# Performance work log

Hardware: AMD Instinct MI355X
Metric: run time of the kernel (lower is better)

## Reference

```python
import jax, jax.numpy as jnp
import numpy as np

STRIDE = 32
ANCHOR_SCALES = (16, 32, 64)
RATIOS = (0.5, 1.0, 2.0)
BASE_SIZE = 16
A = 9                    # base_anchors
PRE_NMS_TOP_N = 6000
POST_NMS_TOP_N = 1000
NMS_THRESH = 0.7
MIN_SIZE = 16.0


def _base_anchors():
    w = h = float(BASE_SIZE)
    cx = cy = (BASE_SIZE - 1) * 0.5
    out = []
    for r in RATIOS:
        ws = np.round(np.sqrt(w * h / r))
        hs = np.round(ws * r)
        for s in ANCHOR_SCALES:
            W_, H_ = ws * s, hs * s
            out.append([cx - 0.5 * (W_ - 1), cy - 0.5 * (H_ - 1),
                        cx + 0.5 * (W_ - 1), cy + 0.5 * (H_ - 1)])
    return np.asarray(out, dtype=np.float32)  # [9,4]


def _conv(x, w, b, padding):
    y = jax.lax.conv_general_dilated(x, w, (1, 1), padding,
                                     dimension_numbers=('NCHW', 'OIHW', 'NCHW'))
    return y + b[None, :, None, None]


def reference(features, rpn_w, rpn_b, cls_w, cls_b, box_w, box_b, image_height, image_width):
    H, W = features.shape[2], features.shape[3]
    x = jax.nn.relu(_conv(features, rpn_w, rpn_b, 'SAME'))
    cls_score = _conv(x, cls_w, cls_b, 'VALID')           # [1,2A,H,W]
    cls_prob = jax.nn.softmax(cls_score, axis=1)           # nn.Softmax2d: softmax over all 2A channels
    bbox_pred = _conv(x, box_w, box_b, 'VALID')            # [1,4A,H,W]

    scores = cls_prob[0, A:].transpose(1, 2, 0).reshape(-1)       # fg scores [H*W*A]
    deltas = bbox_pred[0].transpose(1, 2, 0).reshape(-1, 4)        # [H*W*A,4]

    base = jnp.asarray(_base_anchors())
    sx = jnp.arange(W, dtype=jnp.float32) * STRIDE
    sy = jnp.arange(H, dtype=jnp.float32) * STRIDE
    sxx, syy = jnp.meshgrid(sx, sy)                                # [H,W]
    shifts = jnp.stack([sxx, syy, sxx, syy], axis=-1).reshape(-1, 4)
    anchors = (shifts[:, None, :] + base[None, :, :]).reshape(-1, 4)

    # bbox_transform_inv decode
    wa = anchors[:, 2] - anchors[:, 0] + 1.0
    ha = anchors[:, 3] - anchors[:, 1] + 1.0
    cxa = anchors[:, 0] + 0.5 * (wa - 1.0)
    cya = anchors[:, 1] + 0.5 * (ha - 1.0)
    cx = deltas[:, 0] * wa + cxa
    cy = deltas[:, 1] * ha + cya
    pw = wa * jnp.exp(deltas[:, 2])
    ph = ha * jnp.exp(deltas[:, 3])
    x1 = jnp.clip(cx - 0.5 * pw, 0.0, image_width - 1.0)
    y1 = jnp.clip(cy - 0.5 * ph, 0.0, image_height - 1.0)
    x2 = jnp.clip(cx + 0.5 * pw, 0.0, image_width - 1.0)
    y2 = jnp.clip(cy + 0.5 * ph, 0.0, image_height - 1.0)
    boxes = jnp.stack([x1, y1, x2, y2], axis=-1)

    valid0 = ((x2 - x1 + 1.0) >= MIN_SIZE) & ((y2 - y1 + 1.0) >= MIN_SIZE)
    scores = jnp.where(valid0, scores, -jnp.inf)

    top_scores, top_idx = jax.lax.top_k(scores, PRE_NMS_TOP_N)
    tb = boxes[top_idx]                                             # [P,4]
    tx1, ty1, tx2, ty2 = tb[:, 0], tb[:, 1], tb[:, 2], tb[:, 3]
    areas = (tx2 - tx1 + 1.0) * (ty2 - ty1 + 1.0)
    xx1 = jnp.maximum(tx1[:, None], tx1[None, :])
    yy1 = jnp.maximum(ty1[:, None], ty1[None, :])
    xx2 = jnp.minimum(tx2[:, None], tx2[None, :])
    yy2 = jnp.minimum(ty2[:, None], ty2[None, :])
    inter = jnp.maximum(xx2 - xx1 + 1.0, 0.0) * jnp.maximum(yy2 - yy1 + 1.0, 0.0)
    iou = inter / (areas[:, None] + areas[None, :] - inter)         # [P,P]

    def step(state, _):
        alive, = (state,) if not isinstance(state, tuple) else (None,)
        return state, None

    def nms_step(state, _):
        alive, sel_list = state
        s = jnp.where(alive, top_scores, -jnp.inf)
        j = jnp.argmax(s)
        ok = s[j] > -jnp.inf
        alive = alive & (jnp.take(iou, j, axis=0) <= NMS_THRESH)    # suppresses j too (iou=1)
        return (alive, sel_list), (j.astype(jnp.int32), ok)

    alive0 = jnp.isfinite(top_scores)
    (_, _), (sel, selv) = jax.lax.scan(nms_step, (alive0, 0),
                                       jnp.arange(POST_NMS_TOP_N), length=POST_NMS_TOP_N)

    out_boxes = tb[sel] * selv[:, None].astype(tb.dtype)            # zero-pad invalid slots
    rois = jnp.concatenate([jnp.zeros((POST_NMS_TOP_N, 1), tb.dtype), out_boxes], axis=1)
    return rois                                                     # [POST_NMS_TOP_N, 5]


def setup_inputs() -> dict:
    key = jax.random.key(0)
    ks = jax.random.split(key, 4)
    features = jax.random.normal(ks[0], (1, 256, 128, 128), dtype=jnp.float32)
    rpn_w = 0.01 * jax.random.normal(ks[1], (256, 256, 3, 3), dtype=jnp.float32)
    rpn_b = jnp.zeros((256,), jnp.float32)
    cls_w = 0.01 * jax.random.normal(ks[2], (18, 256, 1, 1), dtype=jnp.float32)
    cls_b = jnp.zeros((18,), jnp.float32)
    box_w = 0.01 * jax.random.normal(ks[3], (36, 256, 1, 1), dtype=jnp.float32)
    box_b = jnp.zeros((36,), jnp.float32)
    return {'features': features, 'rpn_w': rpn_w, 'rpn_b': rpn_b,
            'cls_w': cls_w, 'cls_b': cls_b, 'box_w': box_w, 'box_b': box_b,
            'image_height': 4096, 'image_width': 4096}
```

## Files before the change

### kernel.cpp

```cpp
#include <hip/hip_runtime.h>
#include <stdint.h>
#include <math.h>

typedef unsigned long long u64;
typedef unsigned int u32;
typedef float float4a __attribute__((ext_vector_type(4), aligned(4)));
typedef unsigned long long u64x2 __attribute__((ext_vector_type(2), aligned(16)));

static const size_t OFF_CTL   = 0;
static const size_t OFF_HIST  = 1024;
static const size_t OFF_DOTS  = 1049600;
static const size_t OFF_WCV   = 4588544;
static const size_t OFF_XD    = 6947840;
static const size_t OFF_BOX   = 23725056;
static const size_t OFF_KEYS  = 26084352;
static const size_t OFF_CKEY  = 27264000;
static const size_t OFF_CIDX  = 27313152;
static const size_t OFF_TB    = 27337728;
static const size_t OFF_TSC   = 27433728;
static const size_t OFF_ALIVE = 27458048;
static const size_t OFF_FPAD  = 32067584;
static const size_t OFF_MASKP = OFF_FPAD;

__device__ __forceinline__ float exp_xla(float x) {
    float m = floorf(__fmaf_rn(x, 1.44269504088896341f, 0.5f));
    float r = __fmaf_rn(m, -0.693359375f, x);
    r = __fmaf_rn(m, 2.12194440e-4f, r);
    float r2 = r * r;
    float p = 1.9875691500e-4f;
    p = __fmaf_rn(p, r, 1.3981999507e-3f);
    p = __fmaf_rn(p, r, 8.3334519073e-3f);
    p = __fmaf_rn(p, r, 4.1665795894e-2f);
    p = __fmaf_rn(p, r, 1.6666665459e-1f);
    p = __fmaf_rn(p, r, 5.0000001201e-1f);
    p = __fmaf_rn(p, r2, r);
    p = __fadd_rn(p, 1.0f);
    int mi = (int)m;
    return p * __int_as_float((mi + 127) << 23);
}

__device__ __forceinline__ void gload_lds16(const void* g, void* l) {
    __builtin_amdgcn_global_load_lds(
        (const __attribute__((address_space(1))) void*)g,
        (__attribute__((address_space(3))) void*)l, 16, 0, 0);
}

__global__ void prep_wcv(const float* __restrict__ rpn_w, float* __restrict__ wcv) {
    int t = blockIdx.x * 256 + threadIdx.x;
    if (t >= 589824) return;
    int tap = t / 65536, rem = t % 65536, ic = rem / 256, oc = rem % 256;
    wcv[t] = rpn_w[oc * 2304 + ic * 9 + tap];
}

__global__ void prep_pad(const float* __restrict__ feat, float* __restrict__ featP) {
    int t = blockIdx.x * 256 + threadIdx.x;
    if (t >= 256 * 130 * 132) return;
    int ic = t / 17160, rem = t % 17160, y = rem / 132, x = rem % 132;
    int sy = y - 1, sx = x - 1;
    float v = 0.f;
    if (sy >= 0 && sy < 128 && sx >= 0 && sx < 128)
        v = feat[ic * 16384 + sy * 128 + sx];
    featP[t] = v;
}

__global__ __launch_bounds__(256, 2) void conv3x3(const float* __restrict__ featP,
                                                  const float* __restrict__ wcv,
                                                  const float* __restrict__ rpn_b,
                                                  float* __restrict__ xd) {
    __shared__ float sW[8192];
    const int band = blockIdx.x & 7;
    const int slot = blockIdx.x >> 3;
    const int tx = slot & 7, ocb = slot >> 3;
    const int oc0 = ocb * 32;
    const int tid = threadIdx.x;
    const int wid = tid >> 6;
    const int lane = tid & 63;
    const int py = lane >> 2, px0 = (lane & 3) * 4;
    const int gy = band * 16 + py, gx0 = tx * 16 + px0;
    const int ocB = oc0 + wid * 8;
    float acc[4][8];
#pragma unroll
    for (int p = 0; p < 4; ++p)
#pragma unroll
        for (int o = 0; o < 8; ++o) acc[p][o] = 0.f;
#pragma unroll
    for (int tap = 0; tap < 9; ++tap) {
        __syncthreads();
        for (int idx = tid; idx < 8192; idx += 256)
            sW[idx] = wcv[tap * 65536 + (idx >> 5) * 256 + oc0 + (idx & 31)];
        __syncthreads();
        const float* fp = featP + (size_t)(gy + tap / 3) * 132 + (gx0 + tap % 3);
        const float* wl = sW + wid * 8;
#pragma unroll 4
        for (int ic = 0; ic < 256; ++ic) {
            float4a fA = *(const float4a*)(fp + (size_t)ic * 17160);
            float4a w0 = *(const float4a*)(wl + ic * 32);
            float4a w1 = *(const float4a*)(wl + ic * 32 + 4);
#pragma unroll
            for (int p = 0; p < 4; ++p) {
#pragma unroll
                for (int o = 0; o < 4; ++o)
                    acc[p][o] = __fmaf_rn(fA[p], w0[o], acc[p][o]);
#pragma unroll
                for (int o = 0; o < 4; ++o)
                    acc[p][4 + o] = __fmaf_rn(fA[p], w1[o], acc[p][4 + o]);
            }
        }
    }
#pragma unroll
    for (int p = 0; p < 4; ++p) {
        float* op = xd + (size_t)(gy * 128 + gx0 + p) * 256 + ocB;
#pragma unroll
        for (int o = 0; o < 8; ++o) {
            float v = __fadd_rn(acc[p][o], rpn_b[ocB + o]);
            op[o] = v > 0.f ? v : 0.f;
        }
    }
}

__global__ __launch_bounds__(256, 1) void heads_seq(const float* __restrict__ xd,
                                                    const float* __restrict__ cls_w,
                                                    const float* __restrict__ box_w,
                                                    float* __restrict__ dots) {
    __shared__ float sX[4][260];
    const int tid = threadIdx.x;
    const int pix0 = blockIdx.x * 4;
    for (int idx = tid; idx < 1024; idx += 256)
        sX[idx >> 8][idx & 255] = xd[(size_t)(pix0 + (idx >> 8)) * 256 + (idx & 255)];
    __syncthreads();
    if (tid < 216) {
        const int pl = tid / 54, o = tid % 54;
        const float* wr = (o < 18) ? (cls_w + o * 256) : (box_w + (o - 18) * 256);
        const float4* x4 = (const float4*)&sX[pl][0];
        const float4* w4 = (const float4*)wr;
        float acc = 0.f;
        for (int q = 0; q < 64; ++q) {
            float4 xv = x4[q];
            float4 wv = w4[q];
            acc = __fmaf_rn(xv.x, wv.x, acc);
            acc = __fmaf_rn(xv.y, wv.y, acc);
            acc = __fmaf_rn(xv.z, wv.z, acc);
            acc = __fmaf_rn(xv.w, wv.w, acc);
        }
        dots[(size_t)(pix0 + pl) * 54 + o] = acc;
    }
}

__global__ __launch_bounds__(256, 1) void decode(const float* __restrict__ dots,
                                                 const float* __restrict__ cls_b,
                                                 const float* __restrict__ box_b,
                                                 float4* __restrict__ boxes,
                                                 u64* __restrict__ keys) {
    const int pix = blockIdx.x * 256 + threadIdx.x;
    if (pix >= 16384) return;
    const float* dt = dots + (size_t)pix * 54;
    float d[54];
#pragma unroll
    for (int i = 0; i < 54; ++i)
        d[i] = __fadd_rn(dt[i], (i < 18 ? cls_b[i] : box_b[i - 18]));
    float m = d[0];
#pragma unroll
    for (int i = 1; i < 18; ++i) m = fmaxf(m, d[i]);
    float e[18];
#pragma unroll
    for (int i = 0; i < 18; ++i) e[i] = exp_xla(__fsub_rn(d[i], m));
    float s = e[0];
#pragma unroll
    for (int i = 1; i < 18; ++i) s = __fadd_rn(s, e[i]);
    const int y = pix >> 7, x = pix & 127;
    const float shx = (float)(x * 32), shy = (float)(y * 32);
    const float AW[9] = {368.f, 736.f, 1472.f, 256.f, 512.f, 1024.f, 176.f, 352.f, 704.f};
    const float AH[9] = {192.f, 384.f, 768.f, 256.f, 512.f, 1024.f, 352.f, 704.f, 1408.f};
#pragma unroll
    for (int a = 0; a < 9; ++a) {
        float score = e[9 + a] / s;
        float wa = AW[a], ha = AH[a];
        float cxa = __fadd_rn(shx, 7.5f), cya = __fadd_rn(shy, 7.5f);
        float dx = d[18 + 4 * a], dyy = d[19 + 4 * a];
        float dw = d[20 + 4 * a], dh = d[21 + 4 * a];
        float cx = __fadd_rn(__fmul_rn(dx, wa), cxa);
        float cy = __fadd_rn(__fmul_rn(dyy, ha), cya);
        float pw = __fmul_rn(wa, exp_xla(dw));
        float ph = __fmul_rn(ha, exp_xla(dh));
        float hx = __fmul_rn(0.5f, pw), hy = __fmul_rn(0.5f, ph);
        float x1 = fminf(fmaxf(__fsub_rn(cx, hx), 0.f), 4095.f);
        float y1 = fminf(fmaxf(__fsub_rn(cy, hy), 0.f), 4095.f);
        float x2 = fminf(fmaxf(__fadd_rn(cx, hx), 0.f), 4095.f);
        float y2 = fminf(fmaxf(__fadd_rn(cy, hy), 0.f), 4095.f);
        float vw = __fadd_rn(__fsub_rn(x2, x1), 1.0f);
        float vh = __fadd_rn(__fsub_rn(y2, y1), 1.0f);
        bool valid = (vw >= 16.0f) && (vh >= 16.0f);
        int i = pix * 9 + a;
        boxes[i] = make_float4(x1, y1, x2, y2);
        u64 k;
        if (valid) {
            u32 b = __float_as_uint(score);
            k = ((u64)(u32)~(b | 0x80000000u) << 32) | (u32)i;
        } else {
            k = (0xFFFFFFFFULL << 32) | (u32)i;
        }
        keys[i] = k;
    }
}

__global__ __launch_bounds__(256) void hist_scan(const u64* __restrict__ keys,
                                                 u32* __restrict__ ghist,
                                                 u64* pfx, u32* tgt,
                                                 u32* done, int pass) {
    __shared__ u32 lh[256];
    __shared__ u32 lastFlag;
    __shared__ u32 h[256];
    __shared__ u32 incl[256];
    const int t = threadIdx.x;
    lh[t] = 0;
    if (t == 0) lastFlag = 0;
    __syncthreads();
    const u64 pref = *pfx;
    const u32 target0 = (pass == 0) ? 6000u : *tgt;
    const int shift = 56 - 8 * pass;
    for (int i = blockIdx.x * 256 + t; i < 147456; i += 64 * 256) {
        u64 k = keys[i];
        bool match = (pass == 0) || ((k >> (shift + 8)) == pref);
        if (match) atomicAdd(&lh[(u32)(k >> shift) & 0xFFu], 1u);
    }
    __syncthreads();
    if (lh[t]) atomicAdd(&ghist[t], lh[t]);
    __threadfence();
    __syncthreads();
    if (t == 0) {
        u32 prev = atomicAdd(done, 1u);
        if (prev == 63) lastFlag = 1;
    }
    __syncthreads();
    if (!lastFlag) return;
    u32 hv = atomicAdd(&ghist[t], 0u);
    h[t] = hv;
    incl[t] = hv;
    __syncthreads();
    for (int off = 1; off < 256; off <<= 1) {
        u32 v = (t >= off) ? incl[t - off] : 0u;
        __syncthreads();
        incl[t] += v;
        __syncthreads();
    }
    u64 p0 = (pass == 0) ? 0ULL : pref;
    u32 before = incl[t] - h[t];
    if (before < target0 && target0 <= incl[t]) {
        *pfx = (p0 << 8) | (u64)t;
        *tgt = target0 - before;
    }
}

__global__ void compact(const u64* __restrict__ keys, const u64* __restrict__ kstar,
                        u32* count, u64* __restrict__ ckey, u32* __restrict__ cidx) {
    int i = blockIdx.x * 256 + threadIdx.x;
    if (i >= 147456) return;
    u64 k = keys[i];
    if (k <= *kstar) {
        u32 pos = atomicAdd(count, 1u);
        if (pos < 6144) { ckey[pos] = k; cidx[pos] = (u32)(k & 0xFFFFFFFFu); }
    }
}

__global__ __launch_bounds__(256) void rank_scatter(const u64* __restrict__ ckey,
                                                    const u32* __restrict__ cidx,
                                                    const u32* __restrict__ count,
                                                    const float4* __restrict__ boxes,
                                                    float4* __restrict__ tb,
                                                    float* __restrict__ tsc) {
    __shared__ u64 LK[6144];
    int N = (int)*count; if (N > 6144) N = 6144;
    for (int i = threadIdx.x; i < N; i += 256) LK[i] = ckey[i];
    __syncthreads();
    int e = blockIdx.x * 256 + threadIdx.x;
    if (e >= N) return;
    u64 myK = LK[e];
    u32 myI = cidx[e];
    int rank = 0;
    for (int c = 0; c < N; ++c) rank += (LK[c] < myK);
    if (rank < 6000) {
        tb[rank] = boxes[myI];
        u32 hi = (u32)(myK >> 32);
        tsc[rank] = (hi == 0xFFFFFFFFu) ? -__builtin_inff()
                                        : __uint_as_float(~hi & 0x7FFFFFFFu);
    }
}

__global__ void alive_init(const float* __restrict__ tsc, u64* __restrict__ alive0) {
    int r = blockIdx.x * 256 + threadIdx.x;
    bool a = false;
    if (r < 6000) a = tsc[r] > -__builtin_inff();
    u64 b = __ballot(a);
    if ((threadIdx.x & 63) == 0) alive0[r >> 6] = b;
}

__global__ __launch_bounds__(256) void nms_mask(const float4* __restrict__ tb,
                                                u64* __restrict__ mask) {
    int tid = blockIdx.x * 256 + threadIdx.x;
    if (tid >= 6000 * 94) return;
    int j = tid / 94, w = tid % 94;
    float4 bj = tb[j];
    float arJ = __fmul_rn(__fadd_rn(__fsub_rn(bj.z, bj.x), 1.0f),
                          __fadd_rn(__fsub_rn(bj.w, bj.y), 1.0f));
    u64 m = 0;
    int base = w * 64;
#pragma unroll 4
    for (int b = 0; b < 64; ++b) {
        int i = base + b;
        if (i >= 6000) break;
        float4 bi = tb[i];
        float arI = __fmul_rn(__fadd_rn(__fsub_rn(bi.z, bi.x), 1.0f),
                              __fadd_rn(__fsub_rn(bi.w, bi.y), 1.0f));
        float xx1 = fmaxf(bj.x, bi.x), yy1 = fmaxf(bj.y, bi.y);
        float xx2 = fminf(bj.z, bi.z), yy2 = fminf(bj.w, bi.w);
        float ww = fmaxf(__fadd_rn(__fsub_rn(xx2, xx1), 1.0f), 0.0f);
        float hh = fmaxf(__fadd_rn(__fsub_rn(yy2, yy1), 1.0f), 0.0f);
        float inter = __fmul_rn(ww, hh);
        float uni = __fsub_rn(__fadd_rn(arJ, arI), inter);
        float iou = inter / uni;
        if (iou > 0.7f) m |= (1ULL << b);
    }
    mask[(size_t)j * 128 + 2 * (w & 63) + (w >> 6)] = m;
}

__global__ __launch_bounds__(64, 1) void nms_seq(const u64* __restrict__ alive0,
                                                 const u64* __restrict__ mask,
                                                 const float4* __restrict__ tb,
                                                 float* __restrict__ out) {
    __shared__ __align__(16) u64 lwin[2][64 * 128];
    __shared__ u32 sel[1000];
    const int lane = threadIdx.x;
    u64 wl = alive0[lane];
    u64 wh = (lane < 30) ? alive0[64 + lane] : 0ULL;
    int base = -1000000;
    int pbase = -1;
    int cur = 0;
    int k = 0;
    for (; k < 1000; ++k) {
        int j;
        {
            u64 blo = __ballot(wl != 0ULL);
            if (blo) {
                int l = __ffsll((long long)blo) - 1;
                u32 a = __builtin_amdgcn_readlane((u32)wl, l);
                u32 b = __builtin_amdgcn_readlane((u32)(wl >> 32), l);
                u64 w = ((u64)b << 32) | (u64)a;
                j = l * 64 + __ffsll((long long)w) - 1;
            } else {
                u64 bhi = __ballot(wh != 0ULL);
                if (!bhi) break;
                int l = __ffsll((long long)bhi) - 1;
                u32 a = __builtin_amdgcn_readlane((u32)wh, l);
                u32 b = __builtin_amdgcn_readlane((u32)(wh >> 32), l);
                u64 w = ((u64)b << 32) | (u64)a;
                j = (64 + l) * 64 + __ffsll((long long)w) - 1;
            }
        }
        if (lane == 0) sel[k] = (u32)j;
        if (j >= base + 64) {
            if (pbase >= 0 && j < pbase + 64) {
                asm volatile("s_waitcnt vmcnt(0)" ::: "memory");
                cur ^= 1;
                base = pbase;
            } else {
                int js = (j > 5936) ? 5936 : j;
                asm volatile("s_waitcnt vmcnt(0)" ::: "memory");
                const char* gsrc = (const char*)mask + (size_t)js * 1024 + (size_t)lane * 16;
                char* ldst = (char*)&lwin[cur][0];
#pragma unroll
                for (int i = 0; i < 64; ++i)
                    gload_lds16(gsrc + (size_t)i * 1024, ldst + i * 1024);
                base = js;
                asm volatile("s_waitcnt vmcnt(0)" ::: "memory");
            }
            pbase = -1;
            if (base + 64 < 6000) {
                int ps = (base + 64 > 5936) ? 5936 : (base + 64);
                const char* gs2 = (const char*)mask + (size_t)ps * 1024 + (size_t)lane * 16;
                char* ld2 = (char*)&lwin[cur ^ 1][0];
#pragma unroll
                for (int i = 0; i < 64; ++i)
                    gload_lds16(gs2 + (size_t)i * 1024, ld2 + i * 1024);
                pbase = ps;
            }
        }
        const int s = j - base;
        u64x2 rd = *(const u64x2*)&lwin[cur][(size_t)s * 128 + 2 * lane];
        u64 rl = rd.x;
        u64 rh = rd.y;
        wl &= ~rl;
        if (lane < 30) wh &= ~rh;
    }
    __syncthreads();
    for (int r = lane; r < k; r += 64) {
        int j = (int)sel[r];
        float4 bj = tb[j];
        out[r * 5 + 1] = bj.x;
        out[r * 5 + 2] = bj.y;
        out[r * 5 + 3] = bj.z;
        out[r * 5 + 4] = bj.w;
    }
}

extern "C" void kernel_launch(void* const* d_in, const int* in_sizes, int n_in,
                              void* d_out, int out_size, void* d_ws, size_t ws_size,
                              hipStream_t stream) {
    const float *feat = nullptr, *rpn_w = nullptr, *rpn_b = nullptr;
    const float *cls_w = nullptr, *cls_b = nullptr, *box_w = nullptr, *box_b = nullptr;
    for (int i = 0; i < n_in; ++i) {
        switch (in_sizes[i]) {
            case 4194304: feat  = (const float*)d_in[i]; break;
            case 589824:  rpn_w = (const float*)d_in[i]; break;
            case 256:     rpn_b = (const float*)d_in[i]; break;
            case 4608:    cls_w = (const float*)d_in[i]; break;
            case 18:      cls_b = (const float*)d_in[i]; break;
            case 9216:    box_w = (const float*)d_in[i]; break;
            case 36:      box_b = (const float*)d_in[i]; break;
            default: break;
        }
    }

    char* w = (char*)d_ws;
    u64* pfx       = (u64*)(w + OFF_CTL);
    u32* tgt       = (u32*)(w + OFF_CTL + 8);
    u32* ctlCount  = (u32*)(w + OFF_CTL + 12);
    u32* done      = (u32*)(w + OFF_CTL + 16);
    u32* hist      = (u32*)(w + OFF_HIST);
    float* dots    = (float*)(w + OFF_DOTS);
    float* wcv     = (float*)(w + OFF_WCV);
    float* xd      = (float*)(w + OFF_XD);
    float4* boxes  = (float4*)(w + OFF_BOX);
    u64* keys      = (u64*)(w + OFF_KEYS);
    u64* ckey      = (u64*)(w + OFF_CKEY);
    u32* cidx      = (u32*)(w + OFF_CIDX);
    float4* tb     = (float4*)(w + OFF_TB);
    float* tsc     = (float*)(w + OFF_TSC);
    u64* alive0    = (u64*)(w + OFF_ALIVE);
    u64* maskP     = (u64*)(w + OFF_MASKP);
    float* featP   = (float*)(w + OFF_FPAD);

    hipMemsetAsync(d_ws, 0, OFF_HIST + 8 * 256 * 4, stream);
    hipMemsetAsync(d_out, 0, (size_t)out_size * sizeof(float), stream);

    prep_wcv<<<2304, 256, 0, stream>>>(rpn_w, wcv);
    prep_pad<<<17160, 256, 0, stream>>>(feat, featP);
    conv3x3<<<512, 256, 0, stream>>>(featP, wcv, rpn_b, xd);
    heads_seq<<<4096, 256, 0, stream>>>(xd, cls_w, box_w, dots);
    decode<<<64, 256, 0, stream>>>(dots, cls_b, box_b, boxes, keys);
    for (int p = 0; p < 8; ++p)
        hist_scan<<<64, 256, 0, stream>>>(keys, hist + p * 256, pfx, tgt, done + p, p);
    compact<<<576, 256, 0, stream>>>(keys, pfx, ctlCount, ckey, cidx);
    rank_scatter<<<24, 256, 0, stream>>>(ckey, cidx, ctlCount, boxes, tb, tsc);
    alive_init<<<24, 256, 0, stream>>>(tsc, alive0);
    nms_mask<<<2204, 256, 0, stream>>>(tb, maskP);
    nms_seq<<<1, 64, 0, stream>>>(alive0, maskP, tb, (float*)d_out);
}
```

Measured before the change: 904.6 us.

## Fuse head dots with decode, halve radix-select passes, fold alive init into scatter

```diff
diff --git a/kernel.cpp b/kernel.cpp
--- a/kernel.cpp
+++ b/kernel.cpp
@@ -17,7 +17,6 @@
 static const size_t OFF_CKEY  = 27264000;
 static const size_t OFF_CIDX  = 27313152;
 static const size_t OFF_TB    = 27337728;
-static const size_t OFF_TSC   = 27433728;
 static const size_t OFF_ALIVE = 27458048;
 static const size_t OFF_FPAD  = 32067584;
 static const size_t OFF_MASKP = OFF_FPAD;
@@ -118,11 +117,15 @@
     }
 }
 
-__global__ __launch_bounds__(256, 1) void heads_seq(const float* __restrict__ xd,
-                                                    const float* __restrict__ cls_w,
-                                                    const float* __restrict__ box_w,
-                                                    float* __restrict__ dots) {
+__global__ __launch_bounds__(256, 1) void heads_decode(const float* __restrict__ xd,
+                                                       const float* __restrict__ cls_w,
+                                                       const float* __restrict__ box_w,
+                                                       const float* __restrict__ cls_b,
+                                                       const float* __restrict__ box_b,
+                                                       float4* __restrict__ boxes,
+                                                       u64* __restrict__ keys) {
     __shared__ float sX[4][260];
+    __shared__ float sD[4][54];
     const int tid = threadIdx.x;
     const int pix0 = blockIdx.x * 4;
     for (int idx = tid; idx < 1024; idx += 256)
@@ -142,18 +145,13 @@
             acc = __fmaf_rn(xv.z, wv.z, acc);
             acc = __fmaf_rn(xv.w, wv.w, acc);
         }
-        dots[(size_t)(pix0 + pl) * 54 + o] = acc;
-    }
-}
-
-__global__ __launch_bounds__(256, 1) void decode(const float* __restrict__ dots,
-                                                 const float* __restrict__ cls_b,
-                                                 const float* __restrict__ box_b,
-                                                 float4* __restrict__ boxes,
-                                                 u64* __restrict__ keys) {
-    const int pix = blockIdx.x * 256 + threadIdx.x;
-    if (pix >= 16384) return;
-    const float* dt = dots + (size_t)pix * 54;
+        sD[pl][o] = acc;
+    }
+    __syncthreads();
+    if (tid >= 36) return;
+    const int pl = tid / 9, a = tid % 9;
+    const int pix = pix0 + pl;
+    const float* dt = sD[pl];
     float d[54];
 #pragma unroll
     for (int i = 0; i < 54; ++i)
@@ -171,36 +169,33 @@
     const float shx = (float)(x * 32), shy = (float)(y * 32);
     const float AW[9] = {368.f, 736.f, 1472.f, 256.f, 512.f, 1024.f, 176.f, 352.f, 704.f};
     const float AH[9] = {192.f, 384.f, 768.f, 256.f, 512.f, 1024.f, 352.f, 704.f, 1408.f};
-#pragma unroll
-    for (int a = 0; a < 9; ++a) {
-        float score = e[9 + a] / s;
-        float wa = AW[a], ha = AH[a];
-        float cxa = __fadd_rn(shx, 7.5f), cya = __fadd_rn(shy, 7.5f);
-        float dx = d[18 + 4 * a], dyy = d[19 + 4 * a];
-        float dw = d[20 + 4 * a], dh = d[21 + 4 * a];
-        float cx = __fadd_rn(__fmul_rn(dx, wa), cxa);
-        float cy = __fadd_rn(__fmul_rn(dyy, ha), cya);
-        float pw = __fmul_rn(wa, exp_xla(dw));
-        float ph = __fmul_rn(ha, exp_xla(dh));
-        float hx = __fmul_rn(0.5f, pw), hy = __fmul_rn(0.5f, ph);
-        float x1 = fminf(fmaxf(__fsub_rn(cx, hx), 0.f), 4095.f);
-        float y1 = fminf(fmaxf(__fsub_rn(cy, hy), 0.f), 4095.f);
-        float x2 = fminf(fmaxf(__fadd_rn(cx, hx), 0.f), 4095.f);
-        float y2 = fminf(fmaxf(__fadd_rn(cy, hy), 0.f), 4095.f);
-        float vw = __fadd_rn(__fsub_rn(x2, x1), 1.0f);
-        float vh = __fadd_rn(__fsub_rn(y2, y1), 1.0f);
-        bool valid = (vw >= 16.0f) && (vh >= 16.0f);
-        int i = pix * 9 + a;
-        boxes[i] = make_float4(x1, y1, x2, y2);
-        u64 k;
-        if (valid) {
-            u32 b = __float_as_uint(score);
-            k = ((u64)(u32)~(b | 0x80000000u) << 32) | (u32)i;
-        } else {
-            k = (0xFFFFFFFFULL << 32) | (u32)i;
-        }
-        keys[i] = k;
-    }
+    float score = e[9 + a] / s;
+    float wa = AW[a], ha = AH[a];
+    float cxa = __fadd_rn(shx, 7.5f), cya = __fadd_rn(shy, 7.5f);
+    float dx = d[18 + 4 * a], dyy = d[19 + 4 * a];
+    float dw = d[20 + 4 * a], dh = d[21 + 4 * a];
+    float cx = __fadd_rn(__fmul_rn(dx, wa), cxa);
+    float cy = __fadd_rn(__fmul_rn(dyy, ha), cya);
+    float pw = __fmul_rn(wa, exp_xla(dw));
+    float ph = __fmul_rn(ha, exp_xla(dh));
+    float hx = __fmul_rn(0.5f, pw), hy = __fmul_rn(0.5f, ph);
+    float x1 = fminf(fmaxf(__fsub_rn(cx, hx), 0.f), 4095.f);
+    float y1 = fminf(fmaxf(__fsub_rn(cy, hy), 0.f), 4095.f);
+    float x2 = fminf(fmaxf(__fadd_rn(cx, hx), 0.f), 4095.f);
+    float y2 = fminf(fmaxf(__fadd_rn(cy, hy), 0.f), 4095.f);
+    float vw = __fadd_rn(__fsub_rn(x2, x1), 1.0f);
+    float vh = __fadd_rn(__fsub_rn(y2, y1), 1.0f);
+    bool valid = (vw >= 16.0f) && (vh >= 16.0f);
+    int i = pix * 9 + a;
+    boxes[i] = make_float4(x1, y1, x2, y2);
+    u64 k;
+    if (valid) {
+        u32 b = __float_as_uint(score);
+        k = ((u64)(u32)~(b | 0x80000000u) << 32) | (u32)i;
+    } else {
+        k = (0xFFFFFFFFULL << 32) | (u32)i;
+    }
+    keys[i] = k;
 }
 
 __global__ __launch_bounds__(256) void hist_scan(const u64* __restrict__ keys,
@@ -252,11 +247,13 @@
 }
 
 __global__ void compact(const u64* __restrict__ keys, const u64* __restrict__ kstar,
-                        u32* count, u64* __restrict__ ckey, u32* __restrict__ cidx) {
+                        u32* count, u64* __restrict__ ckey, u32* __restrict__ cidx,
+                        u64* __restrict__ alive0) {
+    if (blockIdx.x == 0 && threadIdx.x < 128) alive0[threadIdx.x] = 0ULL;
     int i = blockIdx.x * 256 + threadIdx.x;
     if (i >= 147456) return;
     u64 k = keys[i];
-    if (k <= *kstar) {
+    if ((k >> 32) <= *kstar) {
         u32 pos = atomicAdd(count, 1u);
         if (pos < 6144) { ckey[pos] = k; cidx[pos] = (u32)(k & 0xFFFFFFFFu); }
     }
@@ -267,7 +264,7 @@
                                                     const u32* __restrict__ count,
                                                     const float4* __restrict__ boxes,
                                                     float4* __restrict__ tb,
-                                                    float* __restrict__ tsc) {
+                                                    u64* __restrict__ alive0) {
     __shared__ u64 LK[6144];
     int N = (int)*count; if (N > 6144) N = 6144;
     for (int i = threadIdx.x; i < N; i += 256) LK[i] = ckey[i];
@@ -280,18 +277,8 @@
     for (int c = 0; c < N; ++c) rank += (LK[c] < myK);
     if (rank < 6000) {
         tb[rank] = boxes[myI];
-        u32 hi = (u32)(myK >> 32);
-        tsc[rank] = (hi == 0xFFFFFFFFu) ? -__builtin_inff()
-                                        : __uint_as_float(~hi & 0x7FFFFFFFu);
-    }
-}
-
-__global__ void alive_init(const float* __restrict__ tsc, u64* __restrict__ alive0) {
-    int r = blockIdx.x * 256 + threadIdx.x;
-    bool a = false;
-    if (r < 6000) a = tsc[r] > -__builtin_inff();
-    u64 b = __ballot(a);
-    if ((threadIdx.x & 63) == 0) alive0[r >> 6] = b;
+        atomicOr(&alive0[rank >> 6], 1ULL << (rank & 63));
+    }
 }
 
 __global__ __launch_bounds__(256) void nms_mask(const float4* __restrict__ tb,
@@ -426,7 +413,6 @@
     u32* ctlCount  = (u32*)(w + OFF_CTL + 12);
     u32* done      = (u32*)(w + OFF_CTL + 16);
     u32* hist      = (u32*)(w + OFF_HIST);
-    float* dots    = (float*)(w + OFF_DOTS);
     float* wcv     = (float*)(w + OFF_WCV);
     float* xd      = (float*)(w + OFF_XD);
     float4* boxes  = (float4*)(w + OFF_BOX);
@@ -434,7 +420,6 @@
     u64* ckey      = (u64*)(w + OFF_CKEY);
     u32* cidx      = (u32*)(w + OFF_CIDX);
     float4* tb     = (float4*)(w + OFF_TB);
-    float* tsc     = (float*)(w + OFF_TSC);
     u64* alive0    = (u64*)(w + OFF_ALIVE);
     u64* maskP     = (u64*)(w + OFF_MASKP);
     float* featP   = (float*)(w + OFF_FPAD);
@@ -445,13 +430,11 @@
     prep_wcv<<<2304, 256, 0, stream>>>(rpn_w, wcv);
     prep_pad<<<17160, 256, 0, stream>>>(feat, featP);
     conv3x3<<<512, 256, 0, stream>>>(featP, wcv, rpn_b, xd);
-    heads_seq<<<4096, 256, 0, stream>>>(xd, cls_w, box_w, dots);
-    decode<<<64, 256, 0, stream>>>(dots, cls_b, box_b, boxes, keys);
-    for (int p = 0; p < 8; ++p)
+    heads_decode<<<4096, 256, 0, stream>>>(xd, cls_w, box_w, cls_b, box_b, boxes, keys);
+    for (int p = 0; p < 4; ++p)
         hist_scan<<<64, 256, 0, stream>>>(keys, hist + p * 256, pfx, tgt, done + p, p);
-    compact<<<576, 256, 0, stream>>>(keys, pfx, ctlCount, ckey, cidx);
-    rank_scatter<<<24, 256, 0, stream>>>(ckey, cidx, ctlCount, boxes, tb, tsc);
-    alive_init<<<24, 256, 0, stream>>>(tsc, alive0);
+    compact<<<576, 256, 0, stream>>>(keys, pfx, ctlCount, ckey, cidx, alive0);
+    rank_scatter<<<24, 256, 0, stream>>>(ckey, cidx, ctlCount, boxes, tb, alive0);
     nms_mask<<<2204, 256, 0, stream>>>(tb, maskP);
     nms_seq<<<1, 64, 0, stream>>>(alive0, maskP, tb, (float*)d_out);
 }
```

Result: no change. 888.2 us (-1.8%).
